# Performance work log

Hardware: AMD Instinct MI355X
Metric: run time of the kernel (lower is better)

The kernel has to match this reference:

```python
import jax, jax.numpy as jnp
import numpy as np

B, D, S, U, H = 2, 1024, 2048, 1024, 16
LN_EPS = 1e-5

def setup_inputs() -> dict:
    key = jax.random.key(0)
    ks = jax.random.split(key, 5)
    std = 0.02
    return {
        "inputs": jax.random.normal(ks[0], (B, D, S), jnp.float32),
        "Wq": jax.random.normal(ks[1], (D, U), jnp.float32) * std,
        "bq": jnp.zeros((U,), jnp.float32),
        "Wk": jax.random.normal(ks[2], (D, U), jnp.float32) * std,
        "bk": jnp.zeros((U,), jnp.float32),
        "Wv": jax.random.normal(ks[3], (D, U), jnp.float32) * std,
        "bv": jnp.zeros((U,), jnp.float32),
        "Wo": jax.random.normal(ks[4], (U, D), jnp.float32) * std,
        "bo": jnp.zeros((D,), jnp.float32),
        "gamma": jnp.ones((D,), jnp.float32),
        "beta": jnp.zeros((D,), jnp.float32),
        "num_heads": H,
    }

def reference(inputs, Wq, bq, Wk, bk, Wv, bv, Wo, bo, gamma, beta, num_heads):
    # inputs: (B, D, S) -> (B, S, D)
    x = jnp.transpose(inputs, (0, 2, 1))
    b, s, d = x.shape

    def proj(W, bias):
        y = jax.nn.relu(x @ W + bias)               # (b, s, U)
        y = y.reshape(b, s, num_heads, -1)
        return jnp.transpose(y, (0, 2, 1, 3))       # (b, h, s, hd)

    Q = proj(Wq, bq)
    K = proj(Wk, bk)
    V = proj(Wv, bv)
    hd = Q.shape[-1]
    scale = 1.0 / np.sqrt(hd).astype(np.float32)

    # Block-wise flash attention in the source is mathematically plain softmax attention
    # (per-block epsilon 1e-10 is negligible); scale applied to Q, no mask, no dropout.
    scores = jnp.einsum('bhid,bhjd->bhij', Q * scale, K)   # (b, h, s, s)
    P = jax.nn.softmax(scores, axis=-1)
    O = jnp.einsum('bhij,bhjd->bhid', P, V)                # (b, h, s, hd)

    O = jnp.transpose(O, (0, 2, 1, 3)).reshape(b, s, -1)   # (b, s, U)
    out = O @ Wo + bo + x                                  # residual add
    mean = jnp.mean(out, axis=-1, keepdims=True)
    var = jnp.var(out, axis=-1, keepdims=True)
    y = (out - mean) * jax.lax.rsqrt(var + LN_EPS) * gamma + beta
    return jnp.transpose(y, (0, 2, 1))                     # (B, D, S)
```

## Files before the change

kernel.cpp:

```cpp
#include <hip/hip_runtime.h>
#include <hip/hip_bf16.h>

typedef __bf16 bf16x8 __attribute__((ext_vector_type(8)));
typedef __bf16 bf16x4 __attribute__((ext_vector_type(4)));
typedef float  f32x4  __attribute__((ext_vector_type(4)));
typedef float  f32x16 __attribute__((ext_vector_type(16)));

#define MFMA16(a, b, c) __builtin_amdgcn_mfma_f32_16x16x32_bf16((a), (b), (c), 0, 0, 0)
#define MFMA32(a, b, c) __builtin_amdgcn_mfma_f32_32x32x16_bf16((a), (b), (c), 0, 0, 0)

namespace {
constexpr int Bb = 2, Dd = 1024, Ss = 2048, Uu = 1024, Hh = 16;
}

#if __has_builtin(__builtin_amdgcn_exp2f)
#define EXP2(x) __builtin_amdgcn_exp2f(x)
#else
#define EXP2(x) __expf((x) * 0.6931471805599453f)
#endif

__device__ __forceinline__ uint32_t pkbf(float a, float b) {
  union { __bf16 h[2]; uint32_t u; } z;
  z.h[0] = (__bf16)a; z.h[1] = (__bf16)b;
  return z.u;
}
#define PLSWAP(a, b) asm("v_permlane32_swap_b32 %0, %1" : "+v"(a), "+v"(b))

__device__ __forceinline__ void gl16(const void* g, void* l) {
  __builtin_amdgcn_global_load_lds((const __attribute__((address_space(1))) uint32_t*)g,
                                   (__attribute__((address_space(3))) uint32_t*)l, 16, 0, 0);
}

#define VMW(n) asm volatile("s_waitcnt vmcnt(" #n ")" ::: "memory")
#define BARRIER_PIN() do { __builtin_amdgcn_s_barrier(); \
  asm volatile("" ::: "memory"); __builtin_amdgcn_sched_barrier(0); } while (0)
#define LGKM0() asm volatile("s_waitcnt lgkmcnt(0)" ::: "memory")

__global__ __launch_bounds__(256) void k_xpose_x(const float* __restrict__ inp,
                                                 __bf16* __restrict__ xb) {
  __shared__ __attribute__((aligned(16))) __bf16 ts[64][72];
  const int s0 = blockIdx.x * 64, d0 = blockIdx.y * 64, b = blockIdx.z;
  const int t = threadIdx.x;
  {
    const int i = t >> 2, c = (t & 3) * 16;
    const float* src = inp + ((size_t)(b * Dd + d0 + i)) * Ss + s0 + c;
#pragma unroll
    for (int q = 0; q < 4; ++q) {
      const float4 f = *(const float4*)(src + q * 4);
      ts[i][c + q * 4 + 0] = (__bf16)f.x;
      ts[i][c + q * 4 + 1] = (__bf16)f.y;
      ts[i][c + q * 4 + 2] = (__bf16)f.z;
      ts[i][c + q * 4 + 3] = (__bf16)f.w;
    }
  }
  __syncthreads();
  {
    const int sl = t >> 2, dc = (t & 3) * 16;
    bf16x8 va, vb;
#pragma unroll
    for (int j = 0; j < 8; ++j) { va[j] = ts[dc + j][sl]; vb[j] = ts[dc + 8 + j][sl]; }
    __bf16* dst = xb + ((size_t)(b * Ss + s0 + sl)) * Dd + d0 + dc;
    *(bf16x8*)dst = va;
    *(bf16x8*)(dst + 8) = vb;
  }
}

__global__ __launch_bounds__(256) void k_xpose_w(const float* __restrict__ w0, const float* __restrict__ w1,
                                                 const float* __restrict__ w2, const float* __restrict__ w3,
                                                 __bf16* __restrict__ o0, __bf16* __restrict__ o1,
                                                 __bf16* __restrict__ o2, __bf16* __restrict__ o3) {
  __shared__ __attribute__((aligned(16))) __bf16 ts[64][72];
  const float* src_m; __bf16* dst_m;
  switch (blockIdx.z) {
    case 0: src_m = w0; dst_m = o0; break;
    case 1: src_m = w1; dst_m = o1; break;
    case 2: src_m = w2; dst_m = o2; break;
    default: src_m = w3; dst_m = o3; break;
  }
  const int n0 = blockIdx.x * 64, k0 = blockIdx.y * 64;
  const int t = threadIdx.x;
  {
    const int i = t >> 2, c = (t & 3) * 16;
    const float* src = src_m + (size_t)(k0 + i) * 1024 + n0 + c;
#pragma unroll
    for (int q = 0; q < 4; ++q) {
      const float4 f = *(const float4*)(src + q * 4);
      ts[i][c + q * 4 + 0] = (__bf16)f.x;
      ts[i][c + q * 4 + 1] = (__bf16)f.y;
      ts[i][c + q * 4 + 2] = (__bf16)f.z;
      ts[i][c + q * 4 + 3] = (__bf16)f.w;
    }
  }
  __syncthreads();
  {
    const int nl = t >> 2, kc = (t & 3) * 16;
    bf16x8 va, vb;
#pragma unroll
    for (int j = 0; j < 8; ++j) { va[j] = ts[kc + j][nl]; vb[j] = ts[kc + 8 + j][nl]; }
    __bf16* dst = dst_m + (size_t)(n0 + nl) * 1024 + k0 + kc;
    *(bf16x8*)dst = va;
    *(bf16x8*)(dst + 8) = vb;
  }
}

__global__ __launch_bounds__(512, 2) void k_gemm_qkv8(const __bf16* __restrict__ A,
    const __bf16* __restrict__ W0, const __bf16* __restrict__ W1, const __bf16* __restrict__ W2,
    const float* __restrict__ b0, const float* __restrict__ b1, const float* __restrict__ b2,
    __bf16* __restrict__ Qb, __bf16* __restrict__ Kb, __bf16* __restrict__ Vt) {
  __shared__ __attribute__((aligned(16))) __bf16 As[4][256][32];
  __shared__ __attribute__((aligned(16))) __bf16 Bs[4][256][32];
  const int t = threadIdx.x;
  const int w = t >> 6, l = t & 63, lg = l >> 4, lr = l & 15;
  const int wm = w >> 2, wn = w & 3;
  const int bid = blockIdx.x;
  const int logical = (bid & 7) * 24 + (bid >> 3);
  const int z = logical >> 6;
  const int rem = logical & 63;
  const int n0 = (rem & 3) * 256, m0 = (rem >> 2) * 256;
  const __bf16* Bt = z == 0 ? W0 : z == 1 ? W1 : W2;
  const float* bias = z == 0 ? b0 : z == 1 ? b1 : b2;

  const int srow = t >> 2, sc8 = t & 3, scol = sc8 * 8;
  const int so = ((sc8 + 4 - ((srow >> 1) & 3)) & 3) * 8;
  const __bf16* gaB = A  + ((size_t)(m0 + srow)) * 1024 + so;
  const __bf16* gbB = Bt + ((size_t)(n0 + srow)) * 1024 + so;
#define STG_A(s, h, kt) gl16(gaB + (size_t)(h) * 128 * 1024 + (kt) * 32, &As[s][(h) * 128 + srow][scol])
#define STG_B(s, h, kt) gl16(gbB + (size_t)(h) * 128 * 1024 + (kt) * 32, &Bs[s][(h) * 128 + srow][scol])

  STG_A(0, 0, 0); STG_A(0, 1, 0); STG_B(0, 0, 0); STG_B(0, 1, 0);
  STG_A(1, 0, 1); STG_A(1, 1, 1); STG_B(1, 0, 1); STG_B(1, 1, 1);
  STG_A(2, 0, 2); STG_A(2, 1, 2); STG_B(2, 0, 2); STG_B(2, 1, 2);
  f32x4 acc[8][4] = {};
  VMW(8);
  BARRIER_PIN();

  const int rdc = ((lg + (lr >> 1)) & 3) * 8;
  const __bf16* Abase = &As[0][0][0] + wm * 4096 + lr * 32 + rdc;
  const __bf16* Bbase = &Bs[0][0][0] + wn * 2048 + lr * 32 + rdc;

  for (int kt = 0; kt < 32; ++kt) {
    const int sC = kt & 3, sS = (kt + 3) & 3;
    const __bf16* Ap = Abase + sC * 8192;
    const __bf16* Bp = Bbase + sC * 8192;
    bf16x8 a0, a1, a2, a3, bb0, bb1, bb2, bb3;
    a0 = *(const bf16x8*)(Ap);         a1 = *(const bf16x8*)(Ap + 512);
    a2 = *(const bf16x8*)(Ap + 1024);  a3 = *(const bf16x8*)(Ap + 1536);
    bb0 = *(const bf16x8*)(Bp);        bb1 = *(const bf16x8*)(Bp + 512);
    bb2 = *(const bf16x8*)(Bp + 1024); bb3 = *(const bf16x8*)(Bp + 1536);
    if (kt < 29) { STG_A(sS, 0, kt + 3); STG_A(sS, 1, kt + 3); }
    BARRIER_PIN();
    LGKM0(); __builtin_amdgcn_sched_barrier(0);
    __builtin_amdgcn_s_setprio(1);
    acc[0][0] = MFMA16(a0, bb0, acc[0][0]); acc[0][1] = MFMA16(a0, bb1, acc[0][1]);
    acc[0][2] = MFMA16(a0, bb2, acc[0][2]); acc[0][3] = MFMA16(a0, bb3, acc[0][3]);
    acc[1][0] = MFMA16(a1, bb0, acc[1][0]); acc[1][1] = MFMA16(a1, bb1, acc[1][1]);
    acc[1][2] = MFMA16(a1, bb2, acc[1][2]); acc[1][3] = MFMA16(a1, bb3, acc[1][3]);
    acc[2][0] = MFMA16(a2, bb0, acc[2][0]); acc[2][1] = MFMA16(a2, bb1, acc[2][1]);
    acc[2][2] = MFMA16(a2, bb2, acc[2][2]); acc[2][3] = MFMA16(a2, bb3, acc[2][3]);
    acc[3][0] = MFMA16(a3, bb0, acc[3][0]); acc[3][1] = MFMA16(a3, bb1, acc[3][1]);
    acc[3][2] = MFMA16(a3, bb2, acc[3][2]); acc[3][3] = MFMA16(a3, bb3, acc[3][3]);
    __builtin_amdgcn_s_setprio(0);
    BARRIER_PIN();
    a0 = *(const bf16x8*)(Ap + 2048);  a1 = *(const bf16x8*)(Ap + 2560);
    a2 = *(const bf16x8*)(Ap + 3072);  a3 = *(const bf16x8*)(Ap + 3584);
    if (kt < 29) { STG_B(sS, 0, kt + 3); STG_B(sS, 1, kt + 3); }
    if (kt < 29) { VMW(8); } else if (kt == 29) { VMW(4); } else if (kt == 30) { VMW(0); }
    BARRIER_PIN();
    LGKM0(); __builtin_amdgcn_sched_barrier(0);
    __builtin_amdgcn_s_setprio(1);
    acc[4][0] = MFMA16(a0, bb0, acc[4][0]); acc[4][1] = MFMA16(a0, bb1, acc[4][1]);
    acc[4][2] = MFMA16(a0, bb2, acc[4][2]); acc[4][3] = MFMA16(a0, bb3, acc[4][3]);
    acc[5][0] = MFMA16(a1, bb0, acc[5][0]); acc[5][1] = MFMA16(a1, bb1, acc[5][1]);
    acc[5][2] = MFMA16(a1, bb2, acc[5][2]); acc[5][3] = MFMA16(a1, bb3, acc[5][3]);
    acc[6][0] = MFMA16(a2, bb0, acc[6][0]); acc[6][1] = MFMA16(a2, bb1, acc[6][1]);
    acc[6][2] = MFMA16(a2, bb2, acc[6][2]); acc[6][3] = MFMA16(a2, bb3, acc[6][3]);
    acc[7][0] = MFMA16(a3, bb0, acc[7][0]); acc[7][1] = MFMA16(a3, bb1, acc[7][1]);
    acc[7][2] = MFMA16(a3, bb2, acc[7][2]); acc[7][3] = MFMA16(a3, bb3, acc[7][3]);
    __builtin_amdgcn_s_setprio(0);
    BARRIER_PIN();
  }
#undef STG_A
#undef STG_B

  const int b = m0 >> 11, sb = m0 & 2047;
  __bf16* Ct = &As[0][0][0];
  float bi[4];
#pragma unroll
  for (int j = 0; j < 4; ++j) bi[j] = bias[n0 + wn * 64 + j * 16 + lr];
  if (z < 2) {
    __bf16* out = z == 0 ? Qb : Kb;
    const float scale = z == 0 ? 0.125f * 1.44269504f : 1.0f;
    const int h0 = n0 >> 6;
    for (int c = 0; c < 4; ++c) {
      __syncthreads();
      if (wm == (c >> 1)) {
        const int q = c & 1;
#pragma unroll
        for (int j = 0; j < 4; ++j) {
          const int nl = wn * 64 + j * 16 + lr;
#pragma unroll
          for (int i2 = 0; i2 < 4; ++i2)
#pragma unroll
            for (int r = 0; r < 4; ++r)
              Ct[(i2 * 16 + lg * 4 + r) * 264 + nl] =
                  (__bf16)(fmaxf(acc[q * 4 + i2][j][r] + bi[j], 0.0f) * scale);
        }
      }
      __syncthreads();
#pragma unroll
      for (int u4 = 0; u4 < 4; ++u4) {
        const int u = u4 * 512 + t;
        const int sl = u >> 5, ru = u & 31;
        const int hh = ru >> 3, sg = ru & 7;
        const bf16x8 v = *(const bf16x8*)&Ct[sl * 264 + hh * 64 + sg * 8];
        *(bf16x8*)(out + ((size_t)(b * Hh + h0 + hh) * Ss + sb + c * 64 + sl) * 64 + sg * 8) = v;
      }
    }
  } else {
    for (int c = 0; c < 4; ++c) {
      __syncthreads();
      if (wn == c) {
#pragma unroll
        for (int j = 0; j < 4; ++j) {
          const int nli = j * 16 + lr;
#pragma unroll
          for (int mi = 0; mi < 8; ++mi)
#pragma unroll
            for (int r2 = 0; r2 < 4; r2 += 2) {
              const int ml = wm * 128 + mi * 16 + lg * 4 + r2;
              const uint32_t pk = pkbf(fmaxf(acc[mi][j][r2] + bi[j], 0.0f),
                                       fmaxf(acc[mi][j][r2 + 1] + bi[j], 0.0f));
              *(uint32_t*)&Ct[nli * 264 + ml] = pk;
            }
        }
      }
      __syncthreads();
#pragma unroll
      for (int u4 = 0; u4 < 4; ++u4) {
        const int u = u4 * 512 + t;
        const int nl = u >> 5, sg = u & 31;
        const bf16x8 v = *(const bf16x8*)&Ct[nl * 264 + sg * 8];
        *(bf16x8*)(Vt + (size_t)(b * 1024 + n0 + c * 64 + nl) * Ss + sb + sg * 8) = v;
      }
    }
  }
}

__device__ __forceinline__ int swz_slot(int row, int slot) { return (slot + (row >> 1)) & 3; }

__device__ __forceinline__ void gemm_core(const __bf16* __restrict__ A, const __bf16* __restrict__ Bt,
                                          __bf16 (*__restrict__ As)[128][32], __bf16 (*__restrict__ Bs)[128][32],
                                          int m0, int n0, int t, f32x4 acc[4][4]) {
  const int w = t >> 6, l = t & 63;
  const int wm = (w >> 1) * 64, wn = (w & 1) * 64;
  const int lg = l >> 4, lr = l & 15;
  const int sr = t >> 2, sc8 = t & 3;
  const int so = ((sc8 + 4 - ((sr >> 1) & 3)) & 3) * 8;
  const __bf16* ga = A + (size_t)(m0 + sr) * 1024 + so;
  const __bf16* gb = Bt + (size_t)(n0 + sr) * 1024 + so;
  const int de = sr * 32 + sc8 * 8;
#define STG(bf, kk) { \
    gl16(ga + (kk) * 32,             &As[bf][0][0] + de); \
    gl16(ga + (kk) * 32 + 64 * 1024, &As[bf][0][0] + de + 64 * 32); \
    gl16(gb + (kk) * 32,             &Bs[bf][0][0] + de); \
    gl16(gb + (kk) * 32 + 64 * 1024, &Bs[bf][0][0] + de + 64 * 32); }
  STG(0, 0) STG(1, 1)
  for (int s = 0; s < 32; ++s) {
    if (s < 31) { VMW(4); } else { VMW(0); }
    BARRIER_PIN();
    if (s + 2 < 32) { const int b2 = (s + 2) % 3; STG(b2, s + 2) }
    const int cb = s % 3;
    bf16x8 af[4], bfr[4];
#pragma unroll
    for (int i = 0; i < 4; ++i) { const int rr = wm + i * 16 + lr; af[i]  = *(const bf16x8*)&As[cb][rr][swz_slot(rr, lg) * 8]; }
#pragma unroll
    for (int i = 0; i < 4; ++i) { const int rr = wn + i * 16 + lr; bfr[i] = *(const bf16x8*)&Bs[cb][rr][swz_slot(rr, lg) * 8]; }
#pragma unroll
    for (int i = 0; i < 4; ++i)
#pragma unroll
      for (int j = 0; j < 4; ++j) acc[i][j] = MFMA16(af[i], bfr[j], acc[i][j]);
  }
#undef STG
}

__global__ __launch_bounds__(256) void k_gemm_o(const __bf16* __restrict__ A, const __bf16* __restrict__ Bt,
                                                const float* __restrict__ bias, const __bf16* __restrict__ xb,
                                                __bf16* __restrict__ Wb, float* __restrict__ partials) {
  __shared__ __attribute__((aligned(16))) char smem[49152];
  auto As = (__bf16 (*)[128][32])smem;
  auto Bs = (__bf16 (*)[128][32])(smem + 24576);
  float* Cs = (float*)smem;
  const int flat = blockIdx.x;
  const int logical = (flat & 7) * 32 + (flat >> 3);
  const int n0 = (logical & 7) * 128, m0 = (logical >> 3) * 128;
  const int t = threadIdx.x, w = t >> 6, l = t & 63;
  const int wm = (w >> 1) * 64, wn = (w & 1) * 64;
  const int lg = l >> 4, lr = l & 15;
  f32x4 acc[4][4] = {};
  gemm_core(A, Bt, As, Bs, m0, n0, t, acc);
  const int sub = t & 31, rid0 = t >> 5;
#pragma unroll
  for (int h2 = 0; h2 < 2; ++h2) {
    __syncthreads();
    if ((w >> 1) == h2) {
#pragma unroll
      for (int j = 0; j < 4; ++j) {
        const int nl = wn + j * 16 + lr;
        const float bi = bias[n0 + nl];
#pragma unroll
        for (int i = 0; i < 4; ++i)
#pragma unroll
          for (int r = 0; r < 4; ++r)
            Cs[(i * 16 + lg * 4 + r) * 132 + nl] = acc[i][j][r] + bi;
      }
    }
    __syncthreads();
#pragma unroll
    for (int p = 0; p < 8; ++p) {
      const int row = p * 8 + rid0;
      const int m = m0 + h2 * 64 + row;
      float4 v = *(const float4*)&Cs[row * 132 + sub * 4];
      const bf16x4 x4 = *(const bf16x4*)&xb[(size_t)m * 1024 + n0 + sub * 4];
      v.x += (float)x4[0]; v.y += (float)x4[1]; v.z += (float)x4[2]; v.w += (float)x4[3];
      bf16x4 pv;
      pv[0] = (__bf16)v.x; pv[1] = (__bf16)v.y; pv[2] = (__bf16)v.z; pv[3] = (__bf16)v.w;
      *(bf16x4*)&Wb[(size_t)m * 1024 + n0 + sub * 4] = pv;
      float s = v.x + v.y + v.z + v.w;
      float q = v.x * v.x + v.y * v.y + v.z * v.z + v.w * v.w;
      s += __shfl_xor(s, 1); s += __shfl_xor(s, 2); s += __shfl_xor(s, 4); s += __shfl_xor(s, 8);
      q += __shfl_xor(q, 1); q += __shfl_xor(q, 2); q += __shfl_xor(q, 4); q += __shfl_xor(q, 8);
      if ((sub & 15) == 0) {
        const int ci = (n0 >> 6) + (sub >> 4);
        partials[((size_t)m * 16 + ci) * 2]     = s;
        partials[((size_t)m * 16 + ci) * 2 + 1] = q;
      }
    }
  }
}

__global__ __launch_bounds__(128, 2) void k_attn7(const __bf16* __restrict__ Qg, const __bf16* __restrict__ Kg,
                                                  const __bf16* __restrict__ Vt, __bf16* __restrict__ Og) {
  __shared__ __attribute__((aligned(16))) __bf16 Ks[64][72];
  __shared__ __attribute__((aligned(16))) __bf16 Vs[64][72];
  const int t = threadIdx.x, l = t & 63, w = t >> 6;
  const int ln = l & 31, hi = l >> 5;
  const int bid = blockIdx.x;
  const int orig = (bid & 7) * 128 + (bid >> 3);
  const int bh = orig >> 5, qt = orig & 31;
  const int q0blk = qt * 64;
  const int q0w = q0blk + w * 32;
  const int b = bh >> 4, h = bh & 15;
  const size_t kbase = (size_t)bh * Ss * 64;
  const int srow = t >> 1, sc2 = (t & 1) * 32;
  const __bf16* Kro = Kg + kbase + (size_t)srow * 64 + sc2;
  const __bf16* Vro = Vt + ((size_t)(bh * 64 + srow)) * Ss + sc2;

  bf16x8 qf0, qf1, qf2, qf3;
  {
    const __bf16* qp = Qg + kbase + (size_t)(q0w + ln) * 64 + hi * 8;
    qf0 = *(const bf16x8*)(qp);
    qf1 = *(const bf16x8*)(qp + 16);
    qf2 = *(const bf16x8*)(qp + 32);
    qf3 = *(const bf16x8*)(qp + 48);
  }
  f32x16 oA = {}, oB = {};
  float lrow = 0.f;

  auto tile_compute = [&]() {
    f32x16 s0 = {}, s1 = {};
    {
      bf16x8 kf;
#define QK(u, cc, sacc) \
      kf = *(const bf16x8*)&Ks[(u) * 32 + ln][(cc) * 16 + hi * 8]; \
      sacc = MFMA32(kf, qf##cc, sacc);
      QK(0, 0, s0) QK(0, 1, s0) QK(0, 2, s0) QK(0, 3, s0)
      QK(1, 0, s1) QK(1, 1, s1) QK(1, 2, s1) QK(1, 3, s1)
#undef QK
    }
#pragma unroll
    for (int r = 0; r < 16; ++r) s0[r] = EXP2(s0[r]);
#pragma unroll
    for (int r = 0; r < 16; ++r) s1[r] = EXP2(s1[r]);
    float sm[16];
#pragma unroll
    for (int r = 0; r < 8; ++r) sm[r] = s0[2 * r] + s0[2 * r + 1];
#pragma unroll
    for (int r = 0; r < 8; ++r) sm[8 + r] = s1[2 * r] + s1[2 * r + 1];
#pragma unroll
    for (int st = 8; st > 0; st >>= 1)
#pragma unroll
      for (int r = 0; r < st; ++r) sm[r] += sm[r + st];
    lrow += sm[0];
    uint32_t w0[8], w1[8];
#pragma unroll
    for (int k = 0; k < 8; ++k) w0[k] = pkbf(s0[2 * k], s0[2 * k + 1]);
#pragma unroll
    for (int k = 0; k < 8; ++k) w1[k] = pkbf(s1[2 * k], s1[2 * k + 1]);
    PLSWAP(w0[0], w0[2]); PLSWAP(w0[1], w0[3]);
    PLSWAP(w0[4], w0[6]); PLSWAP(w0[5], w0[7]);
    PLSWAP(w1[0], w1[2]); PLSWAP(w1[1], w1[3]);
    PLSWAP(w1[4], w1[6]); PLSWAP(w1[5], w1[7]);
    union U4 { uint32_t u[4]; bf16x8 v; };
    U4 z;
    bf16x8 pa0, pa1, pa2, pa3;
    z.u[0] = w0[0]; z.u[1] = w0[1]; z.u[2] = w0[2]; z.u[3] = w0[3]; pa0 = z.v;
    z.u[0] = w0[4]; z.u[1] = w0[5]; z.u[2] = w0[6]; z.u[3] = w0[7]; pa1 = z.v;
    z.u[0] = w1[0]; z.u[1] = w1[1]; z.u[2] = w1[2]; z.u[3] = w1[3]; pa2 = z.v;
    z.u[0] = w1[4]; z.u[1] = w1[5]; z.u[2] = w1[6]; z.u[3] = w1[7]; pa3 = z.v;
    {
      bf16x8 vf;
#define PV(half, ti, pa, oacc) \
      vf = *(const bf16x8*)&Vs[(half) * 32 + ln][(ti) * 16 + hi * 8]; \
      oacc = MFMA32(vf, pa, oacc);
      PV(0, 0, pa0, oA) PV(0, 1, pa1, oA) PV(0, 2, pa2, oA) PV(0, 3, pa3, oA)
      PV(1, 0, pa0, oB) PV(1, 1, pa1, oB) PV(1, 2, pa2, oB) PV(1, 3, pa3, oB)
#undef PV
    }
  };

  bf16x8 kst[4], vst[4];
#pragma unroll
  for (int u = 0; u < 4; ++u) {
    kst[u] = *(const bf16x8*)(Kro + u * 8);
    vst[u] = *(const bf16x8*)(Vro + u * 8);
  }
  for (int tt = 0; tt < 32; ++tt) {
#pragma unroll
    for (int u = 0; u < 4; ++u) {
      *(bf16x8*)&Ks[srow][sc2 + u * 8] = kst[u];
      *(bf16x8*)&Vs[srow][sc2 + u * 8] = vst[u];
    }
    LGKM0();
    BARRIER_PIN();
    if (tt < 31) {
      const size_t ko = (size_t)(tt + 1) * 64;
#pragma unroll
      for (int u = 0; u < 4; ++u) {
        kst[u] = *(const bf16x8*)(Kro + ko * 64 + u * 8);
        vst[u] = *(const bf16x8*)(Vro + ko + u * 8);
      }
    }
    tile_compute();
    BARRIER_PIN();
  }
  {
    uint32_t a = __builtin_bit_cast(uint32_t, lrow), bsw = a;
    PLSWAP(a, bsw);
    lrow = __builtin_bit_cast(float, a) + __builtin_bit_cast(float, bsw);
  }
  const float rl = 1.0f / lrow;
  __bf16* Os = &Ks[0][0];
  const int ql = w * 32 + ln;
#pragma unroll
  for (int r0 = 0; r0 < 4; ++r0)
#pragma unroll
    for (int j = 0; j < 4; ++j) {
      Os[ql * 68 + hi * 4 + r0 * 8 + j]      = (__bf16)(oA[r0 * 4 + j] * rl);
      Os[ql * 68 + 32 + hi * 4 + r0 * 8 + j] = (__bf16)(oB[r0 * 4 + j] * rl);
    }
  __syncthreads();
  const int sub = t & 7, rid0 = t >> 3;
#pragma unroll
  for (int p = 0; p < 4; ++p) {
    const int rid = p * 16 + rid0;
    const bf16x8 v = *(const bf16x8*)&Os[rid * 68 + sub * 8];
    *(bf16x8*)(Og + ((size_t)(b * Ss + q0blk + rid)) * Uu + h * 64 + sub * 8) = v;
  }
}

__global__ __launch_bounds__(256) void k_ln_stats(const float* __restrict__ partials, float* __restrict__ stats) {
  const int row = blockIdx.x * 256 + threadIdx.x;
  float s = 0.f, q = 0.f;
#pragma unroll
  for (int c = 0; c < 16; ++c) {
    s += partials[((size_t)row * 16 + c) * 2];
    q += partials[((size_t)row * 16 + c) * 2 + 1];
  }
  const float mean = s * (1.0f / 1024.0f);
  const float var = q * (1.0f / 1024.0f) - mean * mean;
  stats[row * 2] = mean;
  stats[row * 2 + 1] = rsqrtf(var + 1e-5f);
}

__global__ __launch_bounds__(256) void k_ln_write(const __bf16* __restrict__ Wb, const float* __restrict__ stats,
                                                  const float* __restrict__ gamma, const float* __restrict__ beta,
                                                  float* __restrict__ out) {
  __shared__ __attribute__((aligned(16))) float ws0[64][65];
  __shared__ float sm[64][2];
  const int d0 = blockIdx.x * 64, s0 = blockIdx.y * 64, b = blockIdx.z;
  const int t = threadIdx.x;
  {
    const int sl = t >> 2, dc = (t & 3) * 16;
    const __bf16* src = Wb + ((size_t)(b * Ss + s0 + sl)) * Dd + d0 + dc;
    const bf16x8 f0 = *(const bf16x8*)src;
    const bf16x8 f1 = *(const bf16x8*)(src + 8);
#pragma unroll
    for (int j = 0; j < 8; ++j) { ws0[dc + j][sl] = (float)f0[j]; ws0[dc + 8 + j][sl] = (float)f1[j]; }
  }
  if (t < 128) sm[t >> 1][t & 1] = stats[(size_t)(b * Ss + s0 + (t >> 1)) * 2 + (t & 1)];
  __syncthreads();
  const int dl = t >> 2, sc = (t & 3) * 16;
  const float g = gamma[d0 + dl], be = beta[d0 + dl];
  float* dst = out + ((size_t)(b * Dd + d0 + dl)) * Ss + s0 + sc;
#pragma unroll
  for (int q = 0; q < 4; ++q) {
    float4 o;
    o.x = (ws0[dl][sc + q * 4 + 0] - sm[sc + q * 4 + 0][0]) * sm[sc + q * 4 + 0][1] * g + be;
    o.y = (ws0[dl][sc + q * 4 + 1] - sm[sc + q * 4 + 1][0]) * sm[sc + q * 4 + 1][1] * g + be;
    o.z = (ws0[dl][sc + q * 4 + 2] - sm[sc + q * 4 + 2][0]) * sm[sc + q * 4 + 2][1] * g + be;
    o.w = (ws0[dl][sc + q * 4 + 3] - sm[sc + q * 4 + 3][0]) * sm[sc + q * 4 + 3][1] * g + be;
    *(float4*)(dst + q * 4) = o;
  }
}

extern "C" void kernel_launch(void* const* d_in, const int* in_sizes, int n_in,
                              void* d_out, int out_size, void* d_ws, size_t ws_size,
                              hipStream_t stream) {
  const float* inp   = (const float*)d_in[0];
  const float* Wq    = (const float*)d_in[1];
  const float* bq    = (const float*)d_in[2];
  const float* Wk    = (const float*)d_in[3];
  const float* bk    = (const float*)d_in[4];
  const float* Wv    = (const float*)d_in[5];
  const float* bv    = (const float*)d_in[6];
  const float* Wo    = (const float*)d_in[7];
  const float* bo    = (const float*)d_in[8];
  const float* gamma = (const float*)d_in[9];
  const float* beta  = (const float*)d_in[10];

  char* ws = (char*)d_ws;
  const size_t MB = 1ull << 20;
  __bf16* xb  = (__bf16*)(ws);
  __bf16* Wqt = (__bf16*)(ws + 8 * MB);
  __bf16* Wkt = (__bf16*)(ws + 10 * MB);
  __bf16* Wvt = (__bf16*)(ws + 12 * MB);
  __bf16* Wot = (__bf16*)(ws + 14 * MB);
  __bf16* Qb  = (__bf16*)(ws + 16 * MB);
  __bf16* Kb  = (__bf16*)(ws + 24 * MB);
  __bf16* Vtb = (__bf16*)(ws + 32 * MB);
  __bf16* Ob  = (__bf16*)(ws + 40 * MB);
  __bf16* Wb  = (__bf16*)(ws + 16 * MB);
  float*  partials = (float*)(ws + 8 * MB);
  float*  stats    = (float*)(ws + 8 * MB + 512 * 1024);

  k_xpose_x<<<dim3(32, 16, 2), 256, 0, stream>>>(inp, xb);
  k_xpose_w<<<dim3(16, 16, 4), 256, 0, stream>>>(Wq, Wk, Wv, Wo, Wqt, Wkt, Wvt, Wot);
  k_gemm_qkv8<<<dim3(192), 512, 0, stream>>>(xb, Wqt, Wkt, Wvt, bq, bk, bv, Qb, Kb, Vtb);
  k_attn7<<<dim3(1024), 128, 0, stream>>>(Qb, Kb, Vtb, Ob);
  k_gemm_o<<<dim3(256), 256, 0, stream>>>(Ob, Wot, bo, xb, Wb, partials);
  k_ln_stats<<<dim3(16), 256, 0, stream>>>(partials, stats);
  k_ln_write<<<dim3(16, 32, 2), 256, 0, stream>>>(Wb, stats, gamma, beta, (float*)d_out);
}
```

Measured before the change: 140.6 us.

## Enlarge attention query tile to 256 rows with double-buffered K/V LDS

The attention kernel now processes 256 query rows per block using 4 waves, each handling 64 rows as two 32-row MFMA groups that share every K/V fragment read from LDS. K/V tiles are double-buffered in LDS, which removes the second barrier per iteration. The intent is to cut global K/V traffic and LDS reads per query row, and to halve barriers. The costs are only 256 blocks on a chip with 256 CUs, a single block per CU, and higher register pressure from doubled accumulators, so latency hiding may suffer.

```diff
diff --git a/kernel.cpp b/kernel.cpp
--- a/kernel.cpp
+++ b/kernel.cpp
@@ -338,131 +338,155 @@
   }
 }
 
-__global__ __launch_bounds__(128, 2) void k_attn7(const __bf16* __restrict__ Qg, const __bf16* __restrict__ Kg,
+__global__ __launch_bounds__(256, 1) void k_attn8(const __bf16* __restrict__ Qg, const __bf16* __restrict__ Kg,
                                                   const __bf16* __restrict__ Vt, __bf16* __restrict__ Og) {
-  __shared__ __attribute__((aligned(16))) __bf16 Ks[64][72];
-  __shared__ __attribute__((aligned(16))) __bf16 Vs[64][72];
+  __shared__ __attribute__((aligned(16))) char smem[36864];
+  auto Ks = (__bf16 (*)[64][72])smem;
+  auto Vs = (__bf16 (*)[64][72])(smem + 18432);
   const int t = threadIdx.x, l = t & 63, w = t >> 6;
   const int ln = l & 31, hi = l >> 5;
   const int bid = blockIdx.x;
-  const int orig = (bid & 7) * 128 + (bid >> 3);
-  const int bh = orig >> 5, qt = orig & 31;
-  const int q0blk = qt * 64;
-  const int q0w = q0blk + w * 32;
+  const int orig = (bid & 7) * 32 + (bid >> 3);
+  const int bh = orig >> 3, qt = orig & 7;
+  const int q0blk = qt * 256;
+  const int q0w = q0blk + w * 64;
   const int b = bh >> 4, h = bh & 15;
   const size_t kbase = (size_t)bh * Ss * 64;
-  const int srow = t >> 1, sc2 = (t & 1) * 32;
-  const __bf16* Kro = Kg + kbase + (size_t)srow * 64 + sc2;
-  const __bf16* Vro = Vt + ((size_t)(bh * 64 + srow)) * Ss + sc2;
-
-  bf16x8 qf0, qf1, qf2, qf3;
-  {
-    const __bf16* qp = Qg + kbase + (size_t)(q0w + ln) * 64 + hi * 8;
-    qf0 = *(const bf16x8*)(qp);
-    qf1 = *(const bf16x8*)(qp + 16);
-    qf2 = *(const bf16x8*)(qp + 32);
-    qf3 = *(const bf16x8*)(qp + 48);
-  }
-  f32x16 oA = {}, oB = {};
-  float lrow = 0.f;
-
-  auto tile_compute = [&]() {
-    f32x16 s0 = {}, s1 = {};
-    {
-      bf16x8 kf;
-#define QK(u, cc, sacc) \
-      kf = *(const bf16x8*)&Ks[(u) * 32 + ln][(cc) * 16 + hi * 8]; \
-      sacc = MFMA32(kf, qf##cc, sacc);
-      QK(0, 0, s0) QK(0, 1, s0) QK(0, 2, s0) QK(0, 3, s0)
-      QK(1, 0, s1) QK(1, 1, s1) QK(1, 2, s1) QK(1, 3, s1)
-#undef QK
-    }
-#pragma unroll
-    for (int r = 0; r < 16; ++r) s0[r] = EXP2(s0[r]);
-#pragma unroll
-    for (int r = 0; r < 16; ++r) s1[r] = EXP2(s1[r]);
-    float sm[16];
-#pragma unroll
-    for (int r = 0; r < 8; ++r) sm[r] = s0[2 * r] + s0[2 * r + 1];
-#pragma unroll
-    for (int r = 0; r < 8; ++r) sm[8 + r] = s1[2 * r] + s1[2 * r + 1];
-#pragma unroll
-    for (int st = 8; st > 0; st >>= 1)
-#pragma unroll
-      for (int r = 0; r < st; ++r) sm[r] += sm[r + st];
-    lrow += sm[0];
-    uint32_t w0[8], w1[8];
-#pragma unroll
-    for (int k = 0; k < 8; ++k) w0[k] = pkbf(s0[2 * k], s0[2 * k + 1]);
-#pragma unroll
-    for (int k = 0; k < 8; ++k) w1[k] = pkbf(s1[2 * k], s1[2 * k + 1]);
-    PLSWAP(w0[0], w0[2]); PLSWAP(w0[1], w0[3]);
-    PLSWAP(w0[4], w0[6]); PLSWAP(w0[5], w0[7]);
-    PLSWAP(w1[0], w1[2]); PLSWAP(w1[1], w1[3]);
-    PLSWAP(w1[4], w1[6]); PLSWAP(w1[5], w1[7]);
-    union U4 { uint32_t u[4]; bf16x8 v; };
-    U4 z;
-    bf16x8 pa0, pa1, pa2, pa3;
-    z.u[0] = w0[0]; z.u[1] = w0[1]; z.u[2] = w0[2]; z.u[3] = w0[3]; pa0 = z.v;
-    z.u[0] = w0[4]; z.u[1] = w0[5]; z.u[2] = w0[6]; z.u[3] = w0[7]; pa1 = z.v;
-    z.u[0] = w1[0]; z.u[1] = w1[1]; z.u[2] = w1[2]; z.u[3] = w1[3]; pa2 = z.v;
-    z.u[0] = w1[4]; z.u[1] = w1[5]; z.u[2] = w1[6]; z.u[3] = w1[7]; pa3 = z.v;
-    {
-      bf16x8 vf;
-#define PV(half, ti, pa, oacc) \
-      vf = *(const bf16x8*)&Vs[(half) * 32 + ln][(ti) * 16 + hi * 8]; \
-      oacc = MFMA32(vf, pa, oacc);
-      PV(0, 0, pa0, oA) PV(0, 1, pa1, oA) PV(0, 2, pa2, oA) PV(0, 3, pa3, oA)
-      PV(1, 0, pa0, oB) PV(1, 1, pa1, oB) PV(1, 2, pa2, oB) PV(1, 3, pa3, oB)
-#undef PV
-    }
-  };
-
-  bf16x8 kst[4], vst[4];
-#pragma unroll
-  for (int u = 0; u < 4; ++u) {
-    kst[u] = *(const bf16x8*)(Kro + u * 8);
-    vst[u] = *(const bf16x8*)(Vro + u * 8);
-  }
+  const int srow = t >> 2, scol = (t & 3) * 16;
+  const __bf16* Kro = Kg + kbase + (size_t)srow * 64 + scol;
+  const __bf16* Vro = Vt + ((size_t)(bh * 64 + srow)) * Ss + scol;
+
+  bf16x8 qf0A, qf1A, qf2A, qf3A, qf0B, qf1B, qf2B, qf3B;
+  {
+    const __bf16* qpA = Qg + kbase + (size_t)(q0w + ln) * 64 + hi * 8;
+    qf0A = *(const bf16x8*)(qpA);
+    qf1A = *(const bf16x8*)(qpA + 16);
+    qf2A = *(const bf16x8*)(qpA + 32);
+    qf3A = *(const bf16x8*)(qpA + 48);
+    const __bf16* qpB = qpA + 32 * 64;
+    qf0B = *(const bf16x8*)(qpB);
+    qf1B = *(const bf16x8*)(qpB + 16);
+    qf2B = *(const bf16x8*)(qpB + 32);
+    qf3B = *(const bf16x8*)(qpB + 48);
+  }
+  f32x16 oA0 = {}, oB0 = {}, oA1 = {}, oB1 = {};
+  float lrow0 = 0.f, lrow1 = 0.f;
+
+  bf16x8 kst0 = *(const bf16x8*)(Kro), kst1 = *(const bf16x8*)(Kro + 8);
+  bf16x8 vst0 = *(const bf16x8*)(Vro), vst1 = *(const bf16x8*)(Vro + 8);
+
   for (int tt = 0; tt < 32; ++tt) {
-#pragma unroll
-    for (int u = 0; u < 4; ++u) {
-      *(bf16x8*)&Ks[srow][sc2 + u * 8] = kst[u];
-      *(bf16x8*)&Vs[srow][sc2 + u * 8] = vst[u];
-    }
+    const int c = tt & 1;
+    *(bf16x8*)&Ks[c][srow][scol]     = kst0;
+    *(bf16x8*)&Ks[c][srow][scol + 8] = kst1;
+    *(bf16x8*)&Vs[c][srow][scol]     = vst0;
+    *(bf16x8*)&Vs[c][srow][scol + 8] = vst1;
     LGKM0();
     BARRIER_PIN();
     if (tt < 31) {
       const size_t ko = (size_t)(tt + 1) * 64;
-#pragma unroll
-      for (int u = 0; u < 4; ++u) {
-        kst[u] = *(const bf16x8*)(Kro + ko * 64 + u * 8);
-        vst[u] = *(const bf16x8*)(Vro + ko + u * 8);
-      }
-    }
-    tile_compute();
-    BARRIER_PIN();
-  }
-  {
-    uint32_t a = __builtin_bit_cast(uint32_t, lrow), bsw = a;
+      kst0 = *(const bf16x8*)(Kro + ko * 64);
+      kst1 = *(const bf16x8*)(Kro + ko * 64 + 8);
+      vst0 = *(const bf16x8*)(Vro + ko);
+      vst1 = *(const bf16x8*)(Vro + ko + 8);
+    }
+    f32x16 s0A = {}, s1A = {}, s0B = {}, s1B = {};
+    {
+      bf16x8 kf;
+#define QK2(u, cc, sA, sB) \
+      kf = *(const bf16x8*)&Ks[c][(u) * 32 + ln][(cc) * 16 + hi * 8]; \
+      sA = MFMA32(kf, qf##cc##A, sA); \
+      sB = MFMA32(kf, qf##cc##B, sB);
+      QK2(0, 0, s0A, s0B) QK2(0, 1, s0A, s0B) QK2(0, 2, s0A, s0B) QK2(0, 3, s0A, s0B)
+      QK2(1, 0, s1A, s1B) QK2(1, 1, s1A, s1B) QK2(1, 2, s1A, s1B) QK2(1, 3, s1A, s1B)
+#undef QK2
+    }
+#pragma unroll
+    for (int r = 0; r < 16; ++r) s0A[r] = EXP2(s0A[r]);
+#pragma unroll
+    for (int r = 0; r < 16; ++r) s1A[r] = EXP2(s1A[r]);
+#pragma unroll
+    for (int r = 0; r < 16; ++r) s0B[r] = EXP2(s0B[r]);
+#pragma unroll
+    for (int r = 0; r < 16; ++r) s1B[r] = EXP2(s1B[r]);
+    {
+      float sm[16];
+#pragma unroll
+      for (int r = 0; r < 8; ++r) sm[r] = s0A[2 * r] + s0A[2 * r + 1];
+#pragma unroll
+      for (int r = 0; r < 8; ++r) sm[8 + r] = s1A[2 * r] + s1A[2 * r + 1];
+#pragma unroll
+      for (int st = 8; st > 0; st >>= 1)
+#pragma unroll
+        for (int r = 0; r < st; ++r) sm[r] += sm[r + st];
+      lrow0 += sm[0];
+    }
+    {
+      float sm[16];
+#pragma unroll
+      for (int r = 0; r < 8; ++r) sm[r] = s0B[2 * r] + s0B[2 * r + 1];
+#pragma unroll
+      for (int r = 0; r < 8; ++r) sm[8 + r] = s1B[2 * r] + s1B[2 * r + 1];
+#pragma unroll
+      for (int st = 8; st > 0; st >>= 1)
+#pragma unroll
+        for (int r = 0; r < st; ++r) sm[r] += sm[r + st];
+      lrow1 += sm[0];
+    }
+    bf16x8 pa0A, pa1A, pa2A, pa3A, pa0B, pa1B, pa2B, pa3B;
+#define PACK4(sv0, sv1, p0, p1, p2, p3) { \
+    uint32_t u0[8], u1[8]; \
+    _Pragma("unroll") for (int k2 = 0; k2 < 8; ++k2) u0[k2] = pkbf(sv0[2 * k2], sv0[2 * k2 + 1]); \
+    _Pragma("unroll") for (int k2 = 0; k2 < 8; ++k2) u1[k2] = pkbf(sv1[2 * k2], sv1[2 * k2 + 1]); \
+    PLSWAP(u0[0], u0[2]); PLSWAP(u0[1], u0[3]); PLSWAP(u0[4], u0[6]); PLSWAP(u0[5], u0[7]); \
+    PLSWAP(u1[0], u1[2]); PLSWAP(u1[1], u1[3]); PLSWAP(u1[4], u1[6]); PLSWAP(u1[5], u1[7]); \
+    union UU { uint32_t u[4]; bf16x8 v; } zz; \
+    zz.u[0] = u0[0]; zz.u[1] = u0[1]; zz.u[2] = u0[2]; zz.u[3] = u0[3]; p0 = zz.v; \
+    zz.u[0] = u0[4]; zz.u[1] = u0[5]; zz.u[2] = u0[6]; zz.u[3] = u0[7]; p1 = zz.v; \
+    zz.u[0] = u1[0]; zz.u[1] = u1[1]; zz.u[2] = u1[2]; zz.u[3] = u1[3]; p2 = zz.v; \
+    zz.u[0] = u1[4]; zz.u[1] = u1[5]; zz.u[2] = u1[6]; zz.u[3] = u1[7]; p3 = zz.v; }
+    PACK4(s0A, s1A, pa0A, pa1A, pa2A, pa3A)
+    PACK4(s0B, s1B, pa0B, pa1B, pa2B, pa3B)
+#undef PACK4
+    {
+      bf16x8 vf;
+#define PV2(half, ti, oacc0, oacc1) \
+      vf = *(const bf16x8*)&Vs[c][(half) * 32 + ln][(ti) * 16 + hi * 8]; \
+      oacc0 = MFMA32(vf, pa##ti##A, oacc0); \
+      oacc1 = MFMA32(vf, pa##ti##B, oacc1);
+      PV2(0, 0, oA0, oA1) PV2(0, 1, oA0, oA1) PV2(0, 2, oA0, oA1) PV2(0, 3, oA0, oA1)
+      PV2(1, 0, oB0, oB1) PV2(1, 1, oB0, oB1) PV2(1, 2, oB0, oB1) PV2(1, 3, oB0, oB1)
+#undef PV2
+    }
+  }
+  {
+    uint32_t a = __builtin_bit_cast(uint32_t, lrow0), bsw = a;
     PLSWAP(a, bsw);
-    lrow = __builtin_bit_cast(float, a) + __builtin_bit_cast(float, bsw);
-  }
-  const float rl = 1.0f / lrow;
-  __bf16* Os = &Ks[0][0];
-  const int ql = w * 32 + ln;
+    lrow0 = __builtin_bit_cast(float, a) + __builtin_bit_cast(float, bsw);
+  }
+  {
+    uint32_t a = __builtin_bit_cast(uint32_t, lrow1), bsw = a;
+    PLSWAP(a, bsw);
+    lrow1 = __builtin_bit_cast(float, a) + __builtin_bit_cast(float, bsw);
+  }
+  const float rl0 = 1.0f / lrow0, rl1 = 1.0f / lrow1;
+  __syncthreads();
+  __bf16* Os = (__bf16*)smem;
+  const int ql0 = w * 64 + ln, ql1 = ql0 + 32;
 #pragma unroll
   for (int r0 = 0; r0 < 4; ++r0)
 #pragma unroll
     for (int j = 0; j < 4; ++j) {
-      Os[ql * 68 + hi * 4 + r0 * 8 + j]      = (__bf16)(oA[r0 * 4 + j] * rl);
-      Os[ql * 68 + 32 + hi * 4 + r0 * 8 + j] = (__bf16)(oB[r0 * 4 + j] * rl);
+      Os[ql0 * 68 + hi * 4 + r0 * 8 + j]      = (__bf16)(oA0[r0 * 4 + j] * rl0);
+      Os[ql0 * 68 + 32 + hi * 4 + r0 * 8 + j] = (__bf16)(oB0[r0 * 4 + j] * rl0);
+      Os[ql1 * 68 + hi * 4 + r0 * 8 + j]      = (__bf16)(oA1[r0 * 4 + j] * rl1);
+      Os[ql1 * 68 + 32 + hi * 4 + r0 * 8 + j] = (__bf16)(oB1[r0 * 4 + j] * rl1);
     }
   __syncthreads();
   const int sub = t & 7, rid0 = t >> 3;
 #pragma unroll
-  for (int p = 0; p < 4; ++p) {
-    const int rid = p * 16 + rid0;
+  for (int p = 0; p < 8; ++p) {
+    const int rid = p * 32 + rid0;
     const bf16x8 v = *(const bf16x8*)&Os[rid * 68 + sub * 8];
     *(bf16x8*)(Og + ((size_t)(b * Ss + q0blk + rid)) * Uu + h * 64 + sub * 8) = v;
   }
@@ -546,7 +570,7 @@
   k_xpose_x<<<dim3(32, 16, 2), 256, 0, stream>>>(inp, xb);
   k_xpose_w<<<dim3(16, 16, 4), 256, 0, stream>>>(Wq, Wk, Wv, Wo, Wqt, Wkt, Wvt, Wot);
   k_gemm_qkv8<<<dim3(192), 512, 0, stream>>>(xb, Wqt, Wkt, Wvt, bq, bk, bv, Qb, Kb, Vtb);
-  k_attn7<<<dim3(1024), 128, 0, stream>>>(Qb, Kb, Vtb, Ob);
+  k_attn8<<<dim3(256), 256, 0, stream>>>(Qb, Kb, Vtb, Ob);
   k_gemm_o<<<dim3(256), 256, 0, stream>>>(Ob, Wot, bo, xb, Wb, partials);
   k_ln_stats<<<dim3(16), 256, 0, stream>>>(partials, stats);
   k_ln_write<<<dim3(16, 32, 2), 256, 0, stream>>>(Wb, stats, gamma, beta, (float*)d_out);
```

After: 137.7 us. -2.1%, faster.
